# Kernel tuning notes

Measured on AMD Instinct MI355X. Metric: run time of the kernel, lower is better.

The kernel has to match this reference:

```python
import jax, jax.numpy as jnp
import numpy as np

B, C, H, W = 4, 64, 64, 64
CQK = C // 8


def setup_inputs() -> dict:
    key = jax.random.key(0)
    ks = jax.random.split(key, 4)
    x = jax.random.normal(ks[0], (B, C, H, W), dtype=jnp.float32)
    Wq = jax.random.normal(ks[1], (CQK, C), dtype=jnp.float32) * (1.0 / np.sqrt(C))
    bq = jnp.zeros((CQK,), dtype=jnp.float32)
    Wk = jax.random.normal(ks[2], (CQK, C), dtype=jnp.float32) * (1.0 / np.sqrt(C))
    bk = jnp.zeros((CQK,), dtype=jnp.float32)
    Wv = jax.random.normal(ks[3], (C, C), dtype=jnp.float32) * (1.0 / np.sqrt(C))
    bv = jnp.zeros((C,), dtype=jnp.float32)
    gamma = jnp.ones((1,), dtype=jnp.float32)
    return {"x": x, "Wq": Wq, "bq": bq, "Wk": Wk, "bk": bk,
            "Wv": Wv, "bv": bv, "gamma": gamma}


def reference(x, Wq, bq, Wk, bk, Wv, bv, gamma):
    b, c, h, w = x.shape
    n = h * w
    xf = x.reshape(b, c, n)                      # [B, C, N]
    # 1x1 convs == per-pixel linear over channels
    q = jnp.einsum('oc,bcn->bon', Wq, xf) + bq[:, None]   # [B, C/8, N]
    k = jnp.einsum('oc,bcn->bon', Wk, xf) + bk[:, None]   # [B, C/8, N]
    v = jnp.einsum('oc,bcn->bon', Wv, xf) + bv[:, None]   # [B, C, N]
    # attention_map[b,i,j] = <q[:, i], k[:, j]>; softmax over j
    attn = jax.nn.softmax(jnp.einsum('bci,bcj->bij', q, k), axis=-1)  # [B, N, N]
    # out[b,c,i] = sum_j v[b,c,j] * attn[b,i,j]  (bmm(V, attn^T))
    out = jnp.einsum('bcj,bij->bci', v, attn).reshape(b, c, h, w)
    return gamma * out + x
```

## Files before the change

### kernel.cpp

```cpp
#include <hip/hip_runtime.h>
#include <hip/hip_bf16.h>
#include <math.h>

#define NPIX 4096

typedef __attribute__((ext_vector_type(8))) short s8;
typedef __attribute__((ext_vector_type(4))) float f4;

static __device__ __forceinline__ unsigned packbf2(float a, float b) {
    union { __hip_bfloat162 h; unsigned u; } x;
    x.h = __float22bfloat162_rn(make_float2(a, b));
    return x.u;
}
static __device__ __forceinline__ float2 unpackbf2(unsigned u) {
    float lo = __uint_as_float(u << 16);
    float hi = __uint_as_float(u & 0xffff0000u);
    return make_float2(lo, hi);
}

__global__ __launch_bounds__(512) void prep_kernel(
    const float* __restrict__ x,
    const float* __restrict__ Wq, const float* __restrict__ bq,
    const float* __restrict__ Wk, const float* __restrict__ bk,
    __hip_bfloat16* __restrict__ qbf, __hip_bfloat16* __restrict__ kbf,
    __hip_bfloat16* __restrict__ xbf)
{
    __shared__ float Xp[64][65];
    int t = threadIdx.x;
    int lane = t & 63;
    int grp  = t >> 6;
    int b  = blockIdx.x >> 6;
    int n0 = (blockIdx.x & 63) << 6;

    const float* xb = x + ((size_t)b << 18);
    __hip_bfloat16* xbb = xbf + ((size_t)b << 18);
#pragma unroll
    for (int u = 0; u < 8; ++u) {
        int c = grp + u * 8;
        float v = xb[((size_t)c << 12) + n0 + lane];
        Xp[c][lane] = v;
        xbb[((size_t)c << 12) + n0 + lane] = __float2bfloat16(v);
    }
    __syncthreads();

    float qa = bq[grp], ka = bk[grp];
    const float* wq = Wq + grp * 64;
    const float* wk = Wk + grp * 64;
#pragma unroll
    for (int c = 0; c < 64; ++c) {
        float xv = Xp[c][lane];
        qa = fmaf(wq[c], xv, qa);
        ka = fmaf(wk[c], xv, ka);
    }
    qa *= 1.4426950408889634f;
    int pix = b * NPIX + n0 + lane;
    qbf[(size_t)pix * 8 + grp] = __float2bfloat16(qa);
    kbf[(size_t)pix * 8 + grp] = __float2bfloat16(ka);
}

__global__ __launch_bounds__(256, 3) void flash_part_kernel(
    const __hip_bfloat16* __restrict__ qbf, const __hip_bfloat16* __restrict__ kbf,
    const __hip_bfloat16* __restrict__ xbf,
    __hip_bfloat16* __restrict__ Opart, float* __restrict__ Lp)
{
    __shared__ __align__(16) char pool[37888];
    unsigned short* Xs = (unsigned short*)pool;

    int t = threadIdx.x;
    int w    = t >> 6;
    int lane = t & 63;
    int quad = lane >> 4;
    int c16  = lane & 15;
    unsigned short* PTw = (unsigned short*)(pool + 17408 + w * 5120);

    int blk  = blockIdx.x;
    int sId  = blk >> 8;
    int rest = blk & 255;
    int b    = rest >> 6;
    int i0   = (rest & 63) << 6;
    int jbase = sId << 10;

    const s8 zero8 = {0, 0, 0, 0, 0, 0, 0, 0};
    const f4 zero4 = {0.f, 0.f, 0.f, 0.f};

    s8 qf[4];
#pragma unroll
    for (int it = 0; it < 4; ++it) {
        s8 qv = *(const s8*)(qbf + ((size_t)(b * NPIX + i0 + it * 16 + c16) << 3));
        qf[it] = (quad == 0) ? qv : zero8;
    }

    f4 acc[4][4];
    float l[4] = {0.f, 0.f, 0.f, 0.f};
#pragma unroll
    for (int it = 0; it < 4; ++it)
#pragma unroll
        for (int cm = 0; cm < 4; ++cm) acc[cm][it] = zero4;

    const __hip_bfloat16* kb = kbf + ((size_t)(b * NPIX) << 3);
    const unsigned short* xg = (const unsigned short*)xbf + ((size_t)b << 18);

    for (int tile = 0; tile < 8; ++tile) {
        int j0 = jbase + (tile << 7);

        __syncthreads();
        {
            int c = t >> 2, seg = t & 3;
            const uint4* src = (const uint4*)(xg + ((size_t)c << 12) + j0 + seg * 32);
            uint4* dst = (uint4*)(Xs + c * 136 + seg * 32);
#pragma unroll
            for (int u = 0; u < 4; ++u) dst[u] = src[u];
        }
        s8 kf0 = *(const s8*)(kb + ((size_t)(j0 + w * 32 + c16) << 3));
        s8 kf1 = *(const s8*)(kb + ((size_t)(j0 + w * 32 + 16 + c16) << 3));
        __syncthreads();

#pragma unroll
        for (int it = 0; it < 4; ++it) {
            f4 s0 = __builtin_amdgcn_mfma_f32_16x16x32_bf16(kf0, qf[it], zero4, 0, 0, 0);
            f4 s1 = __builtin_amdgcn_mfma_f32_16x16x32_bf16(kf1, qf[it], zero4, 0, 0, 0);
            float e00 = exp2f(s0[0]), e01 = exp2f(s0[1]);
            float e02 = exp2f(s0[2]), e03 = exp2f(s0[3]);
            float e10 = exp2f(s1[0]), e11 = exp2f(s1[1]);
            float e12 = exp2f(s1[2]), e13 = exp2f(s1[3]);
            l[it] += ((e00 + e01) + (e02 + e03)) + ((e10 + e11) + (e12 + e13));
            int i = it * 16 + c16;
            uint2 pk0, pk1;
            pk0.x = packbf2(e00, e01); pk0.y = packbf2(e02, e03);
            pk1.x = packbf2(e10, e11); pk1.y = packbf2(e12, e13);
            *(uint2*)(PTw + i * 40 + quad * 4) = pk0;
            *(uint2*)(PTw + i * 40 + 16 + quad * 4) = pk1;
        }

        s8 pf[4];
#pragma unroll
        for (int it = 0; it < 4; ++it)
            pf[it] = *(const s8*)(PTw + (it * 16 + c16) * 40 + quad * 8);
#pragma unroll
        for (int cm = 0; cm < 4; ++cm) {
            s8 xf = *(const s8*)(Xs + (cm * 16 + c16) * 136 + w * 32 + quad * 8);
#pragma unroll
            for (int it = 0; it < 4; ++it)
                acc[cm][it] = __builtin_amdgcn_mfma_f32_16x16x32_bf16(xf, pf[it], acc[cm][it], 0, 0, 0);
        }
    }

    float* Osh = (float*)pool;
    float* Lsh = (float*)(pool + 17408);

#pragma unroll
    for (int it = 0; it < 4; ++it) {
        l[it] += __shfl_xor(l[it], 16);
        l[it] += __shfl_xor(l[it], 32);
    }
    __syncthreads();
    if (quad == 0) {
#pragma unroll
        for (int it = 0; it < 4; ++it) Lsh[w * 64 + it * 16 + c16] = l[it];
    }

    for (int wv = 0; wv < 4; ++wv) {
        __syncthreads();
        if (w == wv) {
#pragma unroll
            for (int cm = 0; cm < 4; ++cm)
#pragma unroll
                for (int it = 0; it < 4; ++it) {
                    int i = it * 16 + c16;
                    int c = cm * 16 + quad * 4;
                    float4* dstp = (float4*)(Osh + i * 68 + c);
                    f4 v = acc[cm][it];
                    if (wv == 0) {
                        *dstp = make_float4(v[0], v[1], v[2], v[3]);
                    } else {
                        float4 o = *dstp;
                        *dstp = make_float4(o.x + v[0], o.y + v[1], o.z + v[2], o.w + v[3]);
                    }
                }
        }
    }
    __syncthreads();

    if (t < 64)
        Lp[(size_t)blk * 64 + t] = Lsh[t] + Lsh[64 + t] + Lsh[128 + t] + Lsh[192 + t];

    {
        int i = t >> 2, c0 = (t & 3) << 4;
        const float* src = Osh + i * 68 + c0;
        uint4 lo, hi;
        lo.x = packbf2(src[0], src[1]);   lo.y = packbf2(src[2], src[3]);
        lo.z = packbf2(src[4], src[5]);   lo.w = packbf2(src[6], src[7]);
        hi.x = packbf2(src[8], src[9]);   hi.y = packbf2(src[10], src[11]);
        hi.z = packbf2(src[12], src[13]); hi.w = packbf2(src[14], src[15]);
        uint4* dst = (uint4*)(Opart + (size_t)blk * 4096 + i * 64 + c0);
        dst[0] = lo; dst[1] = hi;
    }
}

__global__ __launch_bounds__(512) void merge_kernel(
    const __hip_bfloat16* __restrict__ Opart, const float* __restrict__ Lp,
    const float* __restrict__ Wv, const float* __restrict__ bv,
    const float* __restrict__ x, const float* __restrict__ gamma,
    float* __restrict__ out)
{
    __shared__ float Osh[64 * 68];
    __shared__ float Wvs[4096];
    __shared__ float LinvS[64];
    __shared__ float bvs[64];

    int t = threadIdx.x;
    int b  = blockIdx.x >> 6;
    int i0 = (blockIdx.x & 63) << 6;

    if (t < 64) {
        int i = t;
        float lt = Lp[(size_t)(0 * 256 + blockIdx.x) * 64 + i]
                 + Lp[(size_t)(1 * 256 + blockIdx.x) * 64 + i]
                 + Lp[(size_t)(2 * 256 + blockIdx.x) * 64 + i]
                 + Lp[(size_t)(3 * 256 + blockIdx.x) * 64 + i];
        LinvS[i] = 1.0f / lt;
        bvs[i] = bv[i];
    }
    {
        const float4* wsrc = (const float4*)Wv;
        float4* wdst = (float4*)Wvs;
        wdst[t] = wsrc[t];
        wdst[t + 512] = wsrc[t + 512];
    }
    __syncthreads();

    {
        int i = t >> 3, c0 = (t & 7) << 3;
        float o[8];
#pragma unroll
        for (int k = 0; k < 8; ++k) o[k] = 0.f;
#pragma unroll
        for (int sId = 0; sId < 4; ++sId) {
            size_t base = (size_t)(sId * 256 + blockIdx.x) * 4096 + i * 64 + c0;
            uint4 pk = *(const uint4*)(Opart + base);
            float2 e0 = unpackbf2(pk.x), e1 = unpackbf2(pk.y);
            float2 e2 = unpackbf2(pk.z), e3 = unpackbf2(pk.w);
            o[0] += e0.x; o[1] += e0.y; o[2] += e1.x; o[3] += e1.y;
            o[4] += e2.x; o[5] += e2.y; o[6] += e3.x; o[7] += e3.y;
        }
        float* dst = Osh + i * 68 + c0;
        *(float4*)(dst + 0) = make_float4(o[0], o[1], o[2], o[3]);
        *(float4*)(dst + 4) = make_float4(o[4], o[5], o[6], o[7]);
    }
    __syncthreads();

    {
        int i  = t & 63;
        int cg = t >> 6;
        float inv = LinvS[i];
        float res[8];
#pragma unroll
        for (int k = 0; k < 8; ++k) res[k] = 0.f;
#pragma unroll 4
        for (int cb = 0; cb < 16; ++cb) {
            float4 o = *(const float4*)(Osh + i * 68 + cb * 4);
#pragma unroll
            for (int k = 0; k < 8; ++k) {
                float4 wv4 = *(const float4*)(Wvs + (cg * 8 + k) * 64 + cb * 4);
                res[k] = fmaf(wv4.x, o.x, fmaf(wv4.y, o.y, fmaf(wv4.z, o.z, fmaf(wv4.w, o.w, res[k]))));
            }
        }
        float g = gamma[0];
        const float* xr = x + ((size_t)b << 18) + i0;
        float* outp = out + ((size_t)b << 18) + i0;
#pragma unroll
        for (int k = 0; k < 8; ++k) {
            int c = cg * 8 + k;
            float attn = fmaf(res[k], inv, bvs[c]);
            size_t off = ((size_t)c << 12) + i;
            outp[off] = fmaf(g, attn, xr[off]);
        }
    }
}

extern "C" void kernel_launch(void* const* d_in, const int* in_sizes, int n_in,
                              void* d_out, int out_size, void* d_ws, size_t ws_size,
                              hipStream_t stream) {
    const float* x     = (const float*)d_in[0];
    const float* Wq    = (const float*)d_in[1];
    const float* bq    = (const float*)d_in[2];
    const float* Wk    = (const float*)d_in[3];
    const float* bk    = (const float*)d_in[4];
    const float* Wv    = (const float*)d_in[5];
    const float* bv    = (const float*)d_in[6];
    const float* gamma = (const float*)d_in[7];
    float* out = (float*)d_out;

    __hip_bfloat16* qbf   = (__hip_bfloat16*)d_ws;
    __hip_bfloat16* kbf   = qbf + (size_t)4 * NPIX * 8;
    __hip_bfloat16* xbf   = kbf + (size_t)4 * NPIX * 8;
    __hip_bfloat16* Opart = xbf + (size_t)4 * NPIX * 64;
    float* Lp = (float*)(Opart + (size_t)1024 * 4096);

    prep_kernel<<<256, 512, 0, stream>>>(x, Wq, bq, Wk, bk, qbf, kbf, xbf);
    flash_part_kernel<<<1024, 256, 0, stream>>>(qbf, kbf, xbf, Opart, Lp);
    merge_kernel<<<256, 512, 0, stream>>>(Opart, Lp, Wv, bv, x, gamma, out);
}
```

Before: 118.8 us.

## Share P tile across waves and split PV output by channel instead of key

The exp'd attention tile P is now written to one shared LDS buffer covering all 128 keys. Each wave then computes a 16-channel slice of the output over the full key range, instead of a partial sum over its own 32 keys. This removes the serialized four-pass cross-wave reduction in LDS and cuts the accumulator registers from 16 to 4 f4 per thread, which allows raising the occupancy hint to 4 blocks. The cost is an extra __syncthreads per tile and more LDS fragment loads for P per wave.

```diff
diff --git a/kernel.cpp b/kernel.cpp
--- a/kernel.cpp
+++ b/kernel.cpp
@@ -58,20 +58,20 @@
     kbf[(size_t)pix * 8 + grp] = __float2bfloat16(ka);
 }
 
-__global__ __launch_bounds__(256, 3) void flash_part_kernel(
+__global__ __launch_bounds__(256, 4) void flash_part_kernel(
     const __hip_bfloat16* __restrict__ qbf, const __hip_bfloat16* __restrict__ kbf,
     const __hip_bfloat16* __restrict__ xbf,
     __hip_bfloat16* __restrict__ Opart, float* __restrict__ Lp)
 {
-    __shared__ __align__(16) char pool[37888];
-    unsigned short* Xs = (unsigned short*)pool;
+    __shared__ __align__(16) char pool[34816];
+    unsigned short* Xs  = (unsigned short*)pool;
+    unsigned short* PTs = (unsigned short*)(pool + 17408);
 
     int t = threadIdx.x;
     int w    = t >> 6;
     int lane = t & 63;
     int quad = lane >> 4;
     int c16  = lane & 15;
-    unsigned short* PTw = (unsigned short*)(pool + 17408 + w * 5120);
 
     int blk  = blockIdx.x;
     int sId  = blk >> 8;
@@ -90,12 +90,10 @@
         qf[it] = (quad == 0) ? qv : zero8;
     }
 
-    f4 acc[4][4];
+    f4 acc[4];
     float l[4] = {0.f, 0.f, 0.f, 0.f};
 #pragma unroll
-    for (int it = 0; it < 4; ++it)
-#pragma unroll
-        for (int cm = 0; cm < 4; ++cm) acc[cm][it] = zero4;
+    for (int ic = 0; ic < 4; ++ic) acc[ic] = zero4;
 
     const __hip_bfloat16* kb = kbf + ((size_t)(b * NPIX) << 3);
     const unsigned short* xg = (const unsigned short*)xbf + ((size_t)b << 18);
@@ -128,20 +126,19 @@
             uint2 pk0, pk1;
             pk0.x = packbf2(e00, e01); pk0.y = packbf2(e02, e03);
             pk1.x = packbf2(e10, e11); pk1.y = packbf2(e12, e13);
-            *(uint2*)(PTw + i * 40 + quad * 4) = pk0;
-            *(uint2*)(PTw + i * 40 + 16 + quad * 4) = pk1;
-        }
-
-        s8 pf[4];
-#pragma unroll
-        for (int it = 0; it < 4; ++it)
-            pf[it] = *(const s8*)(PTw + (it * 16 + c16) * 40 + quad * 8);
-#pragma unroll
-        for (int cm = 0; cm < 4; ++cm) {
-            s8 xf = *(const s8*)(Xs + (cm * 16 + c16) * 136 + w * 32 + quad * 8);
-#pragma unroll
-            for (int it = 0; it < 4; ++it)
-                acc[cm][it] = __builtin_amdgcn_mfma_f32_16x16x32_bf16(xf, pf[it], acc[cm][it], 0, 0, 0);
+            *(uint2*)(PTs + i * 136 + w * 32 + quad * 4) = pk0;
+            *(uint2*)(PTs + i * 136 + w * 32 + 16 + quad * 4) = pk1;
+        }
+        __syncthreads();
+
+#pragma unroll
+        for (int kc = 0; kc < 4; ++kc) {
+            s8 xf = *(const s8*)(Xs + (w * 16 + c16) * 136 + kc * 32 + quad * 8);
+#pragma unroll
+            for (int ic = 0; ic < 4; ++ic) {
+                s8 pf = *(const s8*)(PTs + (ic * 16 + c16) * 136 + kc * 32 + quad * 8);
+                acc[ic] = __builtin_amdgcn_mfma_f32_16x16x32_bf16(xf, pf, acc[ic], 0, 0, 0);
+            }
         }
     }
 
@@ -158,26 +155,11 @@
 #pragma unroll
         for (int it = 0; it < 4; ++it) Lsh[w * 64 + it * 16 + c16] = l[it];
     }
-
-    for (int wv = 0; wv < 4; ++wv) {
-        __syncthreads();
-        if (w == wv) {
-#pragma unroll
-            for (int cm = 0; cm < 4; ++cm)
-#pragma unroll
-                for (int it = 0; it < 4; ++it) {
-                    int i = it * 16 + c16;
-                    int c = cm * 16 + quad * 4;
-                    float4* dstp = (float4*)(Osh + i * 68 + c);
-                    f4 v = acc[cm][it];
-                    if (wv == 0) {
-                        *dstp = make_float4(v[0], v[1], v[2], v[3]);
-                    } else {
-                        float4 o = *dstp;
-                        *dstp = make_float4(o.x + v[0], o.y + v[1], o.z + v[2], o.w + v[3]);
-                    }
-                }
-        }
+#pragma unroll
+    for (int ic = 0; ic < 4; ++ic) {
+        f4 v = acc[ic];
+        *(float4*)(Osh + (ic * 16 + c16) * 68 + w * 16 + quad * 4) =
+            make_float4(v[0], v[1], v[2], v[3]);
     }
     __syncthreads();
 
```

Result: faster. 115.0 us (-3.2%).
